# Performance work log

Measured on AMD Instinct MI355X. Metric: run time of the kernel, lower is better.

The kernel has to match this reference:

```python
import jax, jax.numpy as jnp
import numpy as np

H, W = 512, 512          # output image size (RenderLayer h, w)
CHUNK = 16               # faces per scan step in the rasterizer
BIG = 1e30
EPS = 1e-8


def _edge(ax, ay, bx, by, px, py):
    # 2D edge function (signed parallelogram area)
    return (px - ax) * (by - ay) - (py - ay) * (bx - ax)


def _project(v, campos, camrot, focal, princpt):
    # v: [N,V,3] -> camera space and pixel space (x_pix, y_pix, z_cam)
    v_cam = jnp.einsum('nij,nvj->nvi', camrot, v - campos[:, None])
    z = jnp.maximum(v_cam[..., 2:3], EPS)
    xy = jnp.einsum('nij,nvj->nvi', focal, v_cam[..., :2] / z) + princpt[:, None]
    v_pix = jnp.concatenate([xy, v_cam[..., 2:3]], axis=-1)
    return v_cam, v_pix


def _rasterize(v_pix, vi):
    # Z-buffer rasterization: returns per-pixel face index (-1 = background).
    N = v_pix.shape[0]
    F = vi.shape[0]
    px = jnp.arange(W, dtype=v_pix.dtype)[None, None, None, :]
    py = jnp.arange(H, dtype=v_pix.dtype)[None, None, :, None]
    tri = v_pix[:, vi]                       # [N,F,3,3]
    nchunks = F // CHUNK
    tri_c = jnp.moveaxis(tri.reshape(N, nchunks, CHUNK, 3, 3), 1, 0)  # [nc,N,C,3,3]
    base = jnp.arange(nchunks, dtype=jnp.int32) * CHUNK

    def body(carry, xs):
        best_d, best_i = carry
        t, b0 = xs                           # t: [N,C,3,3]
        x0 = t[:, :, 0, 0][..., None, None]; y0 = t[:, :, 0, 1][..., None, None]; z0 = t[:, :, 0, 2][..., None, None]
        x1 = t[:, :, 1, 0][..., None, None]; y1 = t[:, :, 1, 1][..., None, None]; z1 = t[:, :, 1, 2][..., None, None]
        x2 = t[:, :, 2, 0][..., None, None]; y2 = t[:, :, 2, 1][..., None, None]; z2 = t[:, :, 2, 2][..., None, None]
        w0 = _edge(x1, y1, x2, y2, px, py)   # [N,C,H,W]
        w1 = _edge(x2, y2, x0, y0, px, py)
        w2 = _edge(x0, y0, x1, y1, px, py)
        area = _edge(x0, y0, x1, y1, x2, y2)
        inside = (w0 * area >= 0) & (w1 * area >= 0) & (w2 * area >= 0) & (jnp.abs(area) > EPS)
        sa = jnp.where(jnp.abs(area) > EPS, area, 1.0)
        zi = (w0 / sa) / jnp.maximum(z0, EPS) + (w1 / sa) / jnp.maximum(z1, EPS) + (w2 / sa) / jnp.maximum(z2, EPS)
        valid = inside & (z0 > EPS) & (z1 > EPS) & (z2 > EPS) & (zi > EPS)
        d = jnp.where(valid, 1.0 / jnp.maximum(zi, EPS), BIG)
        d_min = jnp.min(d, axis=1)
        i_min = jnp.argmin(d, axis=1).astype(jnp.int32) + b0
        upd = d_min < best_d
        return (jnp.where(upd, d_min, best_d), jnp.where(upd, i_min, best_i)), None

    init = (jnp.full((N, H, W), BIG, v_pix.dtype), jnp.full((N, H, W), -1, jnp.int32))
    (best_d, best_i), _ = jax.lax.scan(body, init, (tri_c, base))
    mask = best_d < BIG
    return jnp.where(mask, best_i, -1), mask


def _interp(v_pix, vt, vi, vti, index_img, mask):
    # Perspective-correct barycentric interp of depth and texcoords (interp_vert_attrs)
    safe = jnp.maximum(index_img, 0)
    f_v = vi[safe]                            # [N,H,W,3]
    f_vt = vti[safe]
    pv = jax.vmap(lambda vp, t: vp[t])(v_pix, f_v)  # [N,H,W,3,3]
    px = jnp.arange(W, dtype=v_pix.dtype)[None, None, :]
    py = jnp.arange(H, dtype=v_pix.dtype)[None, :, None]
    x0, y0 = pv[..., 0, 0], pv[..., 0, 1]
    x1, y1 = pv[..., 1, 0], pv[..., 1, 1]
    x2, y2 = pv[..., 2, 0], pv[..., 2, 1]
    w0 = _edge(x1, y1, x2, y2, px, py)
    w1 = _edge(x2, y2, x0, y0, px, py)
    w2 = _edge(x0, y0, x1, y1, px, py)
    area = _edge(x0, y0, x1, y1, x2, y2)
    sa = jnp.where(jnp.abs(area) > EPS, area, 1.0)
    b = jnp.stack([w0, w1, w2], -1) / sa[..., None]     # screen-space bary [N,H,W,3]
    z = jnp.maximum(pv[..., 2], EPS)
    bz = b / z
    zi = jnp.maximum(jnp.sum(bz, -1, keepdims=True), EPS)
    bary = jnp.where(mask[..., None], bz / zi, 0.0)     # perspective-correct bary
    depth_img = jnp.where(mask, 1.0 / zi[..., 0], 0.0)
    vt_tri = vt[f_vt]                                   # [N,H,W,3,2]
    vt_img = jnp.einsum('nhwk,nhwkc->nhwc', bary, vt_tri)
    return depth_img, bary, vt_img


def _grid_sample_border(tex, grid):
    # torch.nn.functional.grid_sample: bilinear, padding_mode='border', align_corners=False
    N, C, Ht, Wt = tex.shape
    t = jnp.moveaxis(tex, 1, -1)              # [N,Ht,Wt,C]
    ix = (grid[..., 0] + 1.0) * 0.5 * Wt - 0.5
    iy = (grid[..., 1] + 1.0) * 0.5 * Ht - 0.5
    x0 = jnp.floor(ix); y0 = jnp.floor(iy)
    fx = (ix - x0)[..., None]; fy = (iy - y0)[..., None]
    x0i = jnp.clip(x0.astype(jnp.int32), 0, Wt - 1)
    x1i = jnp.clip(x0.astype(jnp.int32) + 1, 0, Wt - 1)
    y0i = jnp.clip(y0.astype(jnp.int32), 0, Ht - 1)
    y1i = jnp.clip(y0.astype(jnp.int32) + 1, 0, Ht - 1)
    gather = jax.vmap(lambda img, y, x: img[y, x])
    v00 = gather(t, y0i, x0i); v01 = gather(t, y0i, x1i)
    v10 = gather(t, y1i, x0i); v11 = gather(t, y1i, x1i)
    out = (v00 * (1 - fx) + v01 * fx) * (1 - fy) + (v10 * (1 - fx) + v11 * fx) * fy
    return jnp.moveaxis(out, -1, 1)           # [N,C,H,W]


def setup_inputs() -> dict:
    key = jax.random.key(0)
    ks = jax.random.split(key, 6)
    N, V, F, T = 2, 4096, 2048, 4096
    xy = jax.random.uniform(ks[0], (N, V, 2), minval=-1.0, maxval=1.0)
    z = jax.random.uniform(ks[1], (N, V, 1), minval=2.0, maxval=4.0)
    v = jnp.concatenate([xy, z], -1)
    tex = jax.random.normal(ks[2], (N, 3, 1024, 1024), dtype=jnp.float32)
    vt = jax.random.uniform(ks[3], (T, 2))
    vi = jax.random.randint(ks[4], (F, 3), 0, V, dtype=jnp.int32)
    vti = jax.random.randint(ks[5], (F, 3), 0, T, dtype=jnp.int32)
    campos = jnp.zeros((N, 3), jnp.float32)
    camrot = jnp.tile(jnp.eye(3, dtype=jnp.float32)[None], (N, 1, 1))
    focal = jnp.tile(jnp.array([[512.0, 0.0], [0.0, 512.0]], jnp.float32)[None], (N, 1, 1))
    princpt = jnp.full((N, 2), 256.0, jnp.float32)
    return {"v": v, "tex": tex, "vt": vt, "vi": vi, "vti": vti,
            "campos": campos, "camrot": camrot, "focal": focal, "princpt": princpt}


def reference(v, tex, vt, vi, vti, campos, camrot, focal, princpt):
    vt = vt.at[:, 1].set(1.0 - vt[:, 1])      # flip_uvs=True buffer transform
    v_cam, v_pix = _project(v, campos, camrot, focal, princpt)
    index_img, mask = _rasterize(jax.lax.stop_gradient(v_pix), vi)
    depth_img, bary, vt_img = _interp(v_pix, vt, vi, vti, index_img, mask)
    grid = vt_img * 2.0 - 1.0                 # uv in [0,1] -> grid_sample coords
    render = _grid_sample_border(tex, grid) * mask[:, None].astype(tex.dtype)
    bary_img = jnp.moveaxis(bary, -1, 1)
    return render, mask.astype(jnp.float32), depth_img, vt_img, bary_img, index_img
```

## Files before the change

kernel.cpp:

```cpp
#include <hip/hip_runtime.h>
#include <math.h>

#define EPSD 1e-8
#define EPSF 1e-8f
#define IMG_H 512
#define IMG_W 512
#define TEX_W 1024
#define TEX_H 1024
#define REJ_SLACK 1e-3
#define FULL_THR 16.0
#define TILES_X (IMG_W / 16)
#define TILES_Y (IMG_H / 16)
#define TILES_PER_IMG (TILES_X * TILES_Y)

__global__ __launch_bounds__(256) void k_project(
    const float* __restrict__ v,
    const float* __restrict__ campos,
    const float* __restrict__ camrot,
    const float* __restrict__ focal,
    const float* __restrict__ princpt,
    double* __restrict__ vpixd,
    int N, int V) {
#pragma clang fp contract(off)
  int i = blockIdx.x * blockDim.x + threadIdx.x;
  if (i >= N * V) return;
  int n = i / V;
  const float* vv = v + (size_t)i * 3;
  double ax = (double)vv[0] - (double)campos[n * 3 + 0];
  double ay = (double)vv[1] - (double)campos[n * 3 + 1];
  double az = (double)vv[2] - (double)campos[n * 3 + 2];
  const float* R = camrot + (size_t)n * 9;
  double cx = ((double)R[0] * ax + (double)R[1] * ay) + (double)R[2] * az;
  double cy = ((double)R[3] * ax + (double)R[4] * ay) + (double)R[5] * az;
  double cz = ((double)R[6] * ax + (double)R[7] * ay) + (double)R[8] * az;
  double zz = fmax(cz, EPSD);
  double xd = cx / zz;
  double yd = cy / zz;
  const float* Fc = focal + (size_t)n * 4;
  double px = ((double)Fc[0] * xd + (double)Fc[1] * yd) + (double)princpt[n * 2 + 0];
  double py = ((double)Fc[2] * xd + (double)Fc[3] * yd) + (double)princpt[n * 2 + 1];
  vpixd[(size_t)i * 3 + 0] = px;
  vpixd[(size_t)i * 3 + 1] = py;
  vpixd[(size_t)i * 3 + 2] = cz;
}

__global__ __launch_bounds__(256) void k_setup(
    const double* __restrict__ vpixd,
    const int* __restrict__ vi,
    double2* __restrict__ tri,
    float4* __restrict__ bbox,
    int* __restrict__ counter,
    int N, int V, int F) {
#pragma clang fp contract(off)
  int i = blockIdx.x * blockDim.x + threadIdx.x;
  if (i == 0) counter[0] = 0;
  if (i >= N * F) return;
  int n = i / F;
  int f = i - n * F;
  int i0 = vi[f * 3 + 0], i1 = vi[f * 3 + 1], i2 = vi[f * 3 + 2];
  const double* p0 = vpixd + ((size_t)n * V + i0) * 3;
  const double* p1 = vpixd + ((size_t)n * V + i1) * 3;
  const double* p2 = vpixd + ((size_t)n * V + i2) * 3;
  double x0 = p0[0], y0 = p0[1], z0 = p0[2];
  double x1 = p1[0], y1 = p1[1], z1 = p1[2];
  double x2 = p2[0], y2 = p2[1], z2 = p2[2];
  double A0 = y2 - y1, B0 = x2 - x1;
  double A1 = y0 - y2, B1 = x0 - x2;
  double A2 = y1 - y0, B2 = x1 - x0;
  double area = (x2 - x0) * A2 - (y2 - y0) * B2;
  bool valid = (fabs(area) > EPSD) && (z0 > EPSD) && (z1 > EPSD) && (z2 > EPSD);
  double s = area;
  double EA0 = 0.0, EB0 = 0.0, EC0 = -1.0;
  double EA1 = 0.0, EB1 = 0.0, EC1 = -1.0;
  double EA2 = 0.0, EB2 = 0.0, EC2 = -1.0;
  double P = 0.0, Q = 0.0, S = 0.0;
  if (valid) {
    EA0 = A0 * s; EB0 = -(B0 * s); EC0 = (y1 * B0 - x1 * A0) * s;
    EA1 = A1 * s; EB1 = -(B1 * s); EC1 = (y2 * B1 - x2 * A1) * s;
    EA2 = A2 * s; EB2 = -(B2 * s); EC2 = (y0 * B2 - x0 * A2) * s;
    double s2 = s * s;
    double R0 = 1.0 / (s2 * fmax(z0, EPSD));
    double R1 = 1.0 / (s2 * fmax(z1, EPSD));
    double R2 = 1.0 / (s2 * fmax(z2, EPSD));
    P = EA0 * R0 + EA1 * R1 + EA2 * R2;
    S = EB0 * R0 + EB1 * R1 + EB2 * R2;
    Q = EC0 * R0 + EC1 * R1 + EC2 * R2;
  }
  double2* T = tri + (size_t)i * 6;
  T[0] = make_double2(EA0, EB0);
  T[1] = make_double2(EC0, EA1);
  T[2] = make_double2(EB1, EC1);
  T[3] = make_double2(EA2, EB2);
  T[4] = make_double2(EC2, P);
  T[5] = make_double2(Q, S);
  float mnx = (float)fmin(x0, fmin(x1, x2));
  float mny = (float)fmin(y0, fmin(y1, y2));
  float mxx = (float)fmax(x0, fmax(x1, x2));
  float mxy = (float)fmax(y0, fmax(y1, y2));
  bbox[i] = make_float4(mnx, mny, mxx, mxy);
}

__device__ inline void steal_to_tile(int s, int& tx, int& ty) {
  int k = (int)(__fsqrt_rn((float)s) * 0.5f);
  while (k > 0 && 4 * k * k > s) --k;
  while (4 * (k + 1) * (k + 1) <= s) ++k;
  int o = s - 4 * k * k;
  int L = 2 * k + 2;
  int x0 = TILES_X / 2 - 1 - k, y0 = TILES_Y / 2 - 1 - k;
  int side = o / (L - 1);
  int off = o - side * (L - 1);
  if (side == 0)      { tx = x0 + off;         ty = y0; }
  else if (side == 1) { tx = x0 + L - 1;       ty = y0 + off; }
  else if (side == 2) { tx = x0 + L - 1 - off; ty = y0 + L - 1; }
  else                { tx = x0;               ty = y0 + L - 1 - off; }
}

__global__ __launch_bounds__(256, 2) void k_raster(
    const double2* __restrict__ tri,
    const float4* __restrict__ bbox,
    int* __restrict__ counter,
    const double* __restrict__ vpixd,
    const float* __restrict__ vt,
    const int* __restrict__ vi,
    const int* __restrict__ vti,
    const float* __restrict__ tex,
    float* __restrict__ out,
    int N, int V, int F) {
#pragma clang fp contract(off)
  __shared__ __align__(16) char smem[25600];
  double2* s_tri = (double2*)smem;
  int* s_idx = (int*)(smem + 24576);
  double* zbuf = (double*)smem;
  int* ibuf = (int*)(smem + 8192);
  __shared__ int s_steal;

  int tid = threadIdx.x;
  int w = tid >> 6, lane = tid & 63;
  int xl = lane & 15, yb = (lane >> 4) * 4;
  unsigned long long lmask = (1ull << lane) - 1ull;
  int FQ = (F + 3) >> 2;
  int fbeg = w * FQ;
  int fend = min(F, fbeg + FQ);
  int NR = (fend > fbeg) ? ((fend - fbeg + 63) >> 6) : 0;
  double2* s_tri_w = s_tri + (size_t)w * (64 * 6);
  int* s_idx_w = s_idx + w * 64;
  const int TOT = N * TILES_PER_IMG;
  const int HW = IMG_H * IMG_W;
  const size_t NHW = (size_t)N * HW;
  float* out_render = out;
  float* out_mask = out + 3 * NHW;
  float* out_depth = out + 4 * NHW;
  float* out_vt = out + 5 * NHW;
  float* out_bary = out + 7 * NHW;
  float* out_idx = out + 10 * NHW;

  for (;;) {
    if (tid == 0) s_steal = atomicAdd(counter, 1);
    __syncthreads();
    int s = s_steal;
    if (s >= TOT) break;
    int n = s % N;
    int q = s / N;
    int tx, ty;
    steal_to_tile(q, tx, ty);

    int x = tx * 16 + xl;
    int ytop = ty * 16;
    double px = (double)x;
    double py0 = (double)(ytop + yb);
    float tminx = (float)(tx * 16) - 0.5f;
    float tmaxx = tminx + 16.0f;
    float tminy = (float)ytop - 0.5f;
    float tmaxy = tminy + 16.0f;
    double X0 = (double)(tx * 16), X1 = X0 + 15.0;
    double Y0 = (double)ytop, Y1 = Y0 + 15.0;

    double bz[4];
    int bi[4];
#pragma unroll
    for (int r = 0; r < 4; ++r) { bz[r] = EPSD; bi[r] = -1; }

    const double2* trin = tri + (size_t)n * F * 6;
    const float4* bbn = bbox + (size_t)n * F;

    int cnt = 0;
    auto survLoop = [&]() {
      int last = cnt - 1;
      double2 c0 = s_tri_w[0], c1 = s_tri_w[1], c2 = s_tri_w[2],
              c3 = s_tri_w[3], c4 = s_tri_w[4], c5 = s_tri_w[5];
      int enc = s_idx_w[0];
      for (int u = 0; u < cnt; ++u) {
        int un = min(u + 1, last);
        const double2* Tn = s_tri_w + (size_t)un * 6;
        double2 m0 = Tn[0], m1 = Tn[1], m2 = Tn[2];
        double2 m3 = Tn[3], m4 = Tn[4], m5 = Tn[5];
        int en = s_idx_w[un];
        int e = __builtin_amdgcn_readfirstlane(enc);
        int ti = e & 0x7fffffff;
        double uu = fma(px, c4.y, c5.x);
        double py = py0;
        if (e < 0) {
#pragma unroll
          for (int r = 0; r < 4; ++r) {
            double zi = fma(py, c5.y, uu);
            if (zi > bz[r]) { bz[r] = zi; bi[r] = ti; }
            py += 1.0;
          }
        } else {
          double q0 = fma(px, c0.x, c1.x);
          double q1 = fma(px, c1.y, c2.y);
          double q2 = fma(px, c3.x, c4.x);
#pragma unroll
          for (int r = 0; r < 4; ++r) {
            double W0 = fma(py, c0.y, q0);
            double W1 = fma(py, c2.x, q1);
            double W2 = fma(py, c3.y, q2);
            double zi = fma(py, c5.y, uu);
            int msk = (__double2hiint(W0) | __double2hiint(W1) |
                       __double2hiint(W2)) >> 31;
            zi = __hiloint2double(__double2hiint(zi) | msk, __double2loint(zi));
            if (zi > bz[r]) { bz[r] = zi; bi[r] = ti; }
            py += 1.0;
          }
        }
        c0 = m0; c1 = m1; c2 = m2; c3 = m3; c4 = m4; c5 = m5; enc = en;
      }
    };

    float4 bbB = make_float4(0.f, 0.f, 0.f, 0.f);
    bool bbpA = false;
    double2 A0, A1, A2, A3, A4, A5;
    if (NR > 0) {
      int t0 = fbeg + lane;
      float4 bbA;
      if (t0 < fend) bbA = bbn[t0];
      bbpA = (t0 < fend) &&
             !(bbA.z < tminx || bbA.x > tmaxx || bbA.w < tminy || bbA.y > tmaxy);
      if (bbpA) {
        const double2* T = trin + (size_t)t0 * 6;
        A0 = T[0]; A1 = T[1]; A2 = T[2]; A3 = T[3]; A4 = T[4]; A5 = T[5];
      }
      if (t0 + 64 < fend) bbB = bbn[t0 + 64];
    }
    for (int r = 0; r < NR; ++r) {
      int t = fbeg + (r << 6) + lane;
      if (cnt > 0) survLoop();
      asm volatile("s_waitcnt lgkmcnt(0)" ::: "memory");
      bool surv = false, full = false;
      if (bbpA) {
        double xs0 = (A0.x >= 0.0) ? X1 : X0;
        double ys0 = (A0.y >= 0.0) ? Y1 : Y0;
        double w0M = fma(ys0, A0.y, fma(xs0, A0.x, A1.x));
        double xs1 = (A1.y >= 0.0) ? X1 : X0;
        double ys1 = (A2.x >= 0.0) ? Y1 : Y0;
        double w1M = fma(ys1, A2.x, fma(xs1, A1.y, A2.y));
        double xs2 = (A3.x >= 0.0) ? X1 : X0;
        double ys2 = (A3.y >= 0.0) ? Y1 : Y0;
        double w2M = fma(ys2, A3.y, fma(xs2, A3.x, A4.x));
        surv = (w0M >= -REJ_SLACK) & (w1M >= -REJ_SLACK) & (w2M >= -REJ_SLACK);
        if (surv) {
          double xn0 = (A0.x >= 0.0) ? X0 : X1;
          double yn0 = (A0.y >= 0.0) ? Y0 : Y1;
          double w0m = fma(yn0, A0.y, fma(xn0, A0.x, A1.x));
          double xn1 = (A1.y >= 0.0) ? X0 : X1;
          double yn1 = (A2.x >= 0.0) ? Y0 : Y1;
          double w1m = fma(yn1, A2.x, fma(xn1, A1.y, A2.y));
          double xn2 = (A3.x >= 0.0) ? X0 : X1;
          double yn2 = (A3.y >= 0.0) ? Y0 : Y1;
          double w2m = fma(yn2, A3.y, fma(xn2, A3.x, A4.x));
          full = (w0m >= FULL_THR) & (w1m >= FULL_THR) & (w2m >= FULL_THR);
        }
      }
      unsigned long long m = __ballot(surv);
      cnt = (int)__popcll(m);
      if (surv) {
        int dst = (int)__popcll(m & lmask);
        double2* d = s_tri_w + (size_t)dst * 6;
        d[0] = A0; d[1] = A1; d[2] = A2; d[3] = A3; d[4] = A4; d[5] = A5;
        s_idx_w[dst] = t | (full ? (int)0x80000000 : 0);
      }
      asm volatile("s_waitcnt lgkmcnt(0)" ::: "memory");
      int tn1 = t + 64;
      bool bbpB = (tn1 < fend) &&
                  !(bbB.z < tminx || bbB.x > tmaxx || bbB.w < tminy || bbB.y > tmaxy);
      if (bbpB) {
        const double2* T = trin + (size_t)tn1 * 6;
        A0 = T[0]; A1 = T[1]; A2 = T[2]; A3 = T[3]; A4 = T[4]; A5 = T[5];
      }
      if (tn1 + 64 < fend) bbB = bbn[tn1 + 64];
      bbpA = bbpB;
    }
    if (cnt > 0) survLoop();

    __syncthreads();
#pragma unroll
    for (int r = 0; r < 4; ++r) {
      int pix = (yb + r) * 16 + xl;
      zbuf[w * 256 + pix] = bz[r];
      ibuf[w * 256 + pix] = bi[r];
    }
    __syncthreads();
    {
      int pix = tid;
      double z = zbuf[pix];
      int i = ibuf[pix];
#pragma unroll
      for (int qq = 1; qq < 4; ++qq) {
        double zq = zbuf[qq * 256 + pix];
        int iq = ibuf[qq * 256 + pix];
        bool take = (zq > z) || ((zq == z) && ((unsigned)iq < (unsigned)i));
        if (take) { z = zq; i = iq; }
      }
      int yloc = pix >> 4, xloc = pix & 15;
      int y = ytop + yloc;
      int xg = tx * 16 + xloc;
      int p = y * IMG_W + xg;
      size_t gid = (size_t)n * HW + p;
      out_idx[gid] = (float)i;

      int idx = i;
      if (idx < 0) {
        for (int c = 0; c < 3; ++c) out_render[(size_t)(n * 3 + c) * HW + p] = 0.0f;
        out_mask[gid] = 0.0f;
        out_depth[gid] = 0.0f;
        out_vt[(size_t)gid * 2 + 0] = 0.0f;
        out_vt[(size_t)gid * 2 + 1] = 0.0f;
        for (int k = 0; k < 3; ++k) out_bary[(size_t)(n * 3 + k) * HW + p] = 0.0f;
      } else {
        int f0 = vi[idx * 3 + 0], f1 = vi[idx * 3 + 1], f2 = vi[idx * 3 + 2];
        int t0i = vti[idx * 3 + 0], t1i = vti[idx * 3 + 1], t2i = vti[idx * 3 + 2];
        const double* pv0 = vpixd + ((size_t)n * V + f0) * 3;
        const double* pv1 = vpixd + ((size_t)n * V + f1) * 3;
        const double* pv2 = vpixd + ((size_t)n * V + f2) * 3;
        float x0 = (float)pv0[0], y0 = (float)pv0[1], z0 = (float)pv0[2];
        float x1 = (float)pv1[0], y1 = (float)pv1[1], z1 = (float)pv1[2];
        float x2 = (float)pv2[0], y2 = (float)pv2[1], z2 = (float)pv2[2];
        float pxf = (float)xg, pyf = (float)y;
        float w0 = (pxf - x1) * (y2 - y1) - (pyf - y1) * (x2 - x1);
        float w1 = (pxf - x2) * (y0 - y2) - (pyf - y2) * (x0 - x2);
        float w2 = (pxf - x0) * (y1 - y0) - (pyf - y0) * (x1 - x0);
        float area = (x2 - x0) * (y1 - y0) - (y2 - y0) * (x1 - x0);
        float sa = (fabsf(area) > EPSF) ? area : 1.0f;
        float b0 = w0 / sa, b1 = w1 / sa, b2 = w2 / sa;
        float zz0 = fmaxf(z0, EPSF), zz1 = fmaxf(z1, EPSF), zz2 = fmaxf(z2, EPSF);
        float bz0 = b0 / zz0, bz1 = b1 / zz1, bz2 = b2 / zz2;
        float zi = fmaxf((bz0 + bz1) + bz2, EPSF);
        float r0 = bz0 / zi, r1 = bz1 / zi, r2 = bz2 / zi;
        float depth = 1.0f / zi;
        float u0 = vt[(size_t)t0i * 2 + 0], q0 = 1.0f - vt[(size_t)t0i * 2 + 1];
        float u1 = vt[(size_t)t1i * 2 + 0], q1 = 1.0f - vt[(size_t)t1i * 2 + 1];
        float u2 = vt[(size_t)t2i * 2 + 0], q2 = 1.0f - vt[(size_t)t2i * 2 + 1];
        float vtx = (r0 * u0 + r1 * u1) + r2 * u2;
        float vty = (r0 * q0 + r1 * q1) + r2 * q2;
        float gx = vtx * 2.0f - 1.0f;
        float gy = vty * 2.0f - 1.0f;
        float ix = ((gx + 1.0f) * 0.5f) * (float)TEX_W - 0.5f;
        float iy = ((gy + 1.0f) * 0.5f) * (float)TEX_H - 0.5f;
        float x0f = floorf(ix), y0f = floorf(iy);
        float fx = ix - x0f, fy = iy - y0f;
        int x0i = min(max((int)x0f, 0), TEX_W - 1);
        int x1i = min(max((int)x0f + 1, 0), TEX_W - 1);
        int y0i = min(max((int)y0f, 0), TEX_H - 1);
        int y1i = min(max((int)y0f + 1, 0), TEX_H - 1);
        float omfx = 1.0f - fx, omfy = 1.0f - fy;
        for (int c = 0; c < 3; ++c) {
          const float* tc = tex + (size_t)(n * 3 + c) * TEX_H * TEX_W;
          float v00 = tc[(size_t)y0i * TEX_W + x0i];
          float v01 = tc[(size_t)y0i * TEX_W + x1i];
          float v10 = tc[(size_t)y1i * TEX_W + x0i];
          float v11 = tc[(size_t)y1i * TEX_W + x1i];
          float o = (v00 * omfx + v01 * fx) * omfy + (v10 * omfx + v11 * fx) * fy;
          out_render[(size_t)(n * 3 + c) * HW + p] = o;
        }
        out_mask[gid] = 1.0f;
        out_depth[gid] = depth;
        out_vt[(size_t)gid * 2 + 0] = vtx;
        out_vt[(size_t)gid * 2 + 1] = vty;
        out_bary[(size_t)(n * 3 + 0) * HW + p] = r0;
        out_bary[(size_t)(n * 3 + 1) * HW + p] = r1;
        out_bary[(size_t)(n * 3 + 2) * HW + p] = r2;
      }
    }
  }
}

extern "C" void kernel_launch(void* const* d_in, const int* in_sizes, int n_in,
                              void* d_out, int out_size, void* d_ws, size_t ws_size,
                              hipStream_t stream) {
  const float* v = (const float*)d_in[0];
  const float* tex = (const float*)d_in[1];
  const float* vt = (const float*)d_in[2];
  const int* vi = (const int*)d_in[3];
  const int* vti = (const int*)d_in[4];
  const float* campos = (const float*)d_in[5];
  const float* camrot = (const float*)d_in[6];
  const float* focal = (const float*)d_in[7];
  const float* princpt = (const float*)d_in[8];
  int N = in_sizes[5] / 3;
  int V = in_sizes[0] / (3 * N);
  int F = in_sizes[3] / 3;

  char* wp = (char*)d_ws;
  double* vpixd = (double*)wp;
  wp += sizeof(double) * (size_t)N * V * 3;
  double2* tri = (double2*)wp;
  wp += sizeof(double2) * (size_t)N * F * 6;
  float4* bbox = (float4*)wp;
  wp += sizeof(float4) * (size_t)N * F;
  int* counter = (int*)wp;

  int nv = N * V;
  k_project<<<(nv + 255) / 256, 256, 0, stream>>>(v, campos, camrot, focal,
                                                  princpt, vpixd, N, V);
  int nf = N * F;
  k_setup<<<(nf + 255) / 256, 256, 0, stream>>>(vpixd, vi, tri, bbox, counter,
                                                N, V, F);
  int nblk = 1536;
  int tot = N * TILES_PER_IMG;
  if (nblk > tot) nblk = tot;
  k_raster<<<nblk, 256, 0, stream>>>(tri, bbox, counter, vpixd, vt, vi, vti,
                                     tex, (float*)d_out, N, V, F);
}
```

Before: 169.3 us.

## Broadcast surviving triangles via readlane instead of LDS compaction

Replaces the per-wave LDS compaction of surviving triangles (ballot, popcount scatter to shared memory, then a separate shaded loop) with direct iteration over the ballot mask, pulling each triangle's edge coefficients from the owning lane via readlane into scalar registers. This removes LDS stores, loads and waitcnt stalls and shrinks shared memory, and it prefetches the next batch into separate registers. The cost is many readlane operations per triangle and higher VGPR pressure from the double-buffered coefficients. The raster grid size also drops from 1536 to 1024 blocks.

```diff
diff --git a/kernel.cpp b/kernel.cpp
--- a/kernel.cpp
+++ b/kernel.cpp
@@ -115,6 +115,12 @@
   else                { tx = x0;               ty = y0 + L - 1 - off; }
 }
 
+__device__ inline double rl_d(double v, int l) {
+  int lo = __builtin_amdgcn_readlane(__double2loint(v), l);
+  int hi = __builtin_amdgcn_readlane(__double2hiint(v), l);
+  return __hiloint2double(hi, lo);
+}
+
 __global__ __launch_bounds__(256, 2) void k_raster(
     const double2* __restrict__ tri,
     const float4* __restrict__ bbox,
@@ -127,9 +133,7 @@
     float* __restrict__ out,
     int N, int V, int F) {
 #pragma clang fp contract(off)
-  __shared__ __align__(16) char smem[25600];
-  double2* s_tri = (double2*)smem;
-  int* s_idx = (int*)(smem + 24576);
+  __shared__ __align__(16) char smem[12288];
   double* zbuf = (double*)smem;
   int* ibuf = (int*)(smem + 8192);
   __shared__ int s_steal;
@@ -137,13 +141,10 @@
   int tid = threadIdx.x;
   int w = tid >> 6, lane = tid & 63;
   int xl = lane & 15, yb = (lane >> 4) * 4;
-  unsigned long long lmask = (1ull << lane) - 1ull;
   int FQ = (F + 3) >> 2;
   int fbeg = w * FQ;
   int fend = min(F, fbeg + FQ);
   int NR = (fend > fbeg) ? ((fend - fbeg + 63) >> 6) : 0;
-  double2* s_tri_w = s_tri + (size_t)w * (64 * 6);
-  int* s_idx_w = s_idx + w * 64;
   const int TOT = N * TILES_PER_IMG;
   const int HW = IMG_H * IMG_W;
   const size_t NHW = (size_t)N * HW;
@@ -182,50 +183,6 @@
 
     const double2* trin = tri + (size_t)n * F * 6;
     const float4* bbn = bbox + (size_t)n * F;
-
-    int cnt = 0;
-    auto survLoop = [&]() {
-      int last = cnt - 1;
-      double2 c0 = s_tri_w[0], c1 = s_tri_w[1], c2 = s_tri_w[2],
-              c3 = s_tri_w[3], c4 = s_tri_w[4], c5 = s_tri_w[5];
-      int enc = s_idx_w[0];
-      for (int u = 0; u < cnt; ++u) {
-        int un = min(u + 1, last);
-        const double2* Tn = s_tri_w + (size_t)un * 6;
-        double2 m0 = Tn[0], m1 = Tn[1], m2 = Tn[2];
-        double2 m3 = Tn[3], m4 = Tn[4], m5 = Tn[5];
-        int en = s_idx_w[un];
-        int e = __builtin_amdgcn_readfirstlane(enc);
-        int ti = e & 0x7fffffff;
-        double uu = fma(px, c4.y, c5.x);
-        double py = py0;
-        if (e < 0) {
-#pragma unroll
-          for (int r = 0; r < 4; ++r) {
-            double zi = fma(py, c5.y, uu);
-            if (zi > bz[r]) { bz[r] = zi; bi[r] = ti; }
-            py += 1.0;
-          }
-        } else {
-          double q0 = fma(px, c0.x, c1.x);
-          double q1 = fma(px, c1.y, c2.y);
-          double q2 = fma(px, c3.x, c4.x);
-#pragma unroll
-          for (int r = 0; r < 4; ++r) {
-            double W0 = fma(py, c0.y, q0);
-            double W1 = fma(py, c2.x, q1);
-            double W2 = fma(py, c3.y, q2);
-            double zi = fma(py, c5.y, uu);
-            int msk = (__double2hiint(W0) | __double2hiint(W1) |
-                       __double2hiint(W2)) >> 31;
-            zi = __hiloint2double(__double2hiint(zi) | msk, __double2loint(zi));
-            if (zi > bz[r]) { bz[r] = zi; bi[r] = ti; }
-            py += 1.0;
-          }
-        }
-        c0 = m0; c1 = m1; c2 = m2; c3 = m3; c4 = m4; c5 = m5; enc = en;
-      }
-    };
 
     float4 bbB = make_float4(0.f, 0.f, 0.f, 0.f);
     bool bbpA = false;
@@ -243,9 +200,7 @@
       if (t0 + 64 < fend) bbB = bbn[t0 + 64];
     }
     for (int r = 0; r < NR; ++r) {
-      int t = fbeg + (r << 6) + lane;
-      if (cnt > 0) survLoop();
-      asm volatile("s_waitcnt lgkmcnt(0)" ::: "memory");
+      int tbase = fbeg + (r << 6);
       bool surv = false, full = false;
       if (bbpA) {
         double xs0 = (A0.x >= 0.0) ? X1 : X0;
@@ -272,25 +227,59 @@
         }
       }
       unsigned long long m = __ballot(surv);
-      cnt = (int)__popcll(m);
-      if (surv) {
-        int dst = (int)__popcll(m & lmask);
-        double2* d = s_tri_w + (size_t)dst * 6;
-        d[0] = A0; d[1] = A1; d[2] = A2; d[3] = A3; d[4] = A4; d[5] = A5;
-        s_idx_w[dst] = t | (full ? (int)0x80000000 : 0);
-      }
-      asm volatile("s_waitcnt lgkmcnt(0)" ::: "memory");
-      int tn1 = t + 64;
+      unsigned long long mf = __ballot(surv && full);
+      int tn1 = tbase + 64 + lane;
       bool bbpB = (tn1 < fend) &&
                   !(bbB.z < tminx || bbB.x > tmaxx || bbB.w < tminy || bbB.y > tmaxy);
+      double2 B0, B1, B2, B3, B4, B5;
       if (bbpB) {
         const double2* T = trin + (size_t)tn1 * 6;
-        A0 = T[0]; A1 = T[1]; A2 = T[2]; A3 = T[3]; A4 = T[4]; A5 = T[5];
+        B0 = T[0]; B1 = T[1]; B2 = T[2]; B3 = T[3]; B4 = T[4]; B5 = T[5];
       }
       if (tn1 + 64 < fend) bbB = bbn[tn1 + 64];
+      while (m) {
+        int src = (int)__builtin_ctzll(m);
+        m &= m - 1;
+        int ti = tbase + src;
+        double P = rl_d(A4.y, src);
+        double Qq = rl_d(A5.x, src);
+        double S = rl_d(A5.y, src);
+        double uu = fma(px, P, Qq);
+        if ((mf >> src) & 1ull) {
+          double py = py0;
+#pragma unroll
+          for (int rr = 0; rr < 4; ++rr) {
+            double zi = fma(py, S, uu);
+            if (zi > bz[rr]) { bz[rr] = zi; bi[rr] = ti; }
+            py += 1.0;
+          }
+        } else {
+          double EA0 = rl_d(A0.x, src), EB0 = rl_d(A0.y, src);
+          double EC0 = rl_d(A1.x, src), EA1 = rl_d(A1.y, src);
+          double EB1 = rl_d(A2.x, src), EC1 = rl_d(A2.y, src);
+          double EA2 = rl_d(A3.x, src), EB2 = rl_d(A3.y, src);
+          double EC2 = rl_d(A4.x, src);
+          double q0 = fma(px, EA0, EC0);
+          double q1 = fma(px, EA1, EC1);
+          double q2 = fma(px, EA2, EC2);
+          double py = py0;
+#pragma unroll
+          for (int rr = 0; rr < 4; ++rr) {
+            double W0 = fma(py, EB0, q0);
+            double W1 = fma(py, EB1, q1);
+            double W2 = fma(py, EB2, q2);
+            double zi = fma(py, S, uu);
+            int msk = (__double2hiint(W0) | __double2hiint(W1) |
+                       __double2hiint(W2)) >> 31;
+            zi = __hiloint2double(__double2hiint(zi) | msk, __double2loint(zi));
+            if (zi > bz[rr]) { bz[rr] = zi; bi[rr] = ti; }
+            py += 1.0;
+          }
+        }
+      }
+      A0 = B0; A1 = B1; A2 = B2; A3 = B3; A4 = B4; A5 = B5;
       bbpA = bbpB;
     }
-    if (cnt > 0) survLoop();
 
     __syncthreads();
 #pragma unroll
@@ -415,7 +404,7 @@
   int nf = N * F;
   k_setup<<<(nf + 255) / 256, 256, 0, stream>>>(vpixd, vi, tri, bbox, counter,
                                                 N, V, F);
-  int nblk = 1536;
+  int nblk = 1024;
   int tot = N * TILES_PER_IMG;
   if (nblk > tot) nblk = tot;
   k_raster<<<nblk, 256, 0, stream>>>(tri, bbox, counter, vpixd, vt, vi, vti,
```

After: 168.0 us. No clear change (-0.7%).
